# Performance work log

Hardware: AMD Instinct MI355X
Metric: run time of the kernel (lower is better)

## Reference

```python
import jax, jax.numpy as jnp
import numpy as np

BN_EPS = 1e-5

def _conv3x3(x, w):
    # x: [N,C,H,W], w: [O,I,3,3], stride 1, padding 1, no bias
    return jax.lax.conv_general_dilated(
        x, w, window_strides=(1, 1), padding=((1, 1), (1, 1)),
        dimension_numbers=("NCHW", "OIHW", "NCHW"))

def _batchnorm(x, gamma, beta):
    # training-mode BN: batch statistics over (N,H,W)
    mean = jnp.mean(x, axis=(0, 2, 3), keepdims=True)
    var = jnp.mean(jnp.square(x - mean), axis=(0, 2, 3), keepdims=True)
    inv = jax.lax.rsqrt(var + BN_EPS)
    g = gamma.reshape(1, -1, 1, 1)
    b = beta.reshape(1, -1, 1, 1)
    return (x - mean) * inv * g + b

def setup_inputs() -> dict:
    key = jax.random.key(0)
    ks = jax.random.split(key, 3)
    x = jax.random.normal(ks[0], (32, 64, 128, 128), dtype=jnp.float32)
    # He-style scaled 3x3 conv kernels
    w1 = jax.random.normal(ks[1], (64, 64, 3, 3), dtype=jnp.float32) * (2.0 / (64 * 9)) ** 0.5
    w2 = jax.random.normal(ks[2], (64, 64, 3, 3), dtype=jnp.float32) * (2.0 / (64 * 9)) ** 0.5
    return {
        "x": x, "w1": w1, "w2": w2,
        "bn1_gamma": jnp.ones((64,), jnp.float32),
        "bn1_beta": jnp.zeros((64,), jnp.float32),
        "bn2_gamma": jnp.ones((64,), jnp.float32),
        "bn2_beta": jnp.zeros((64,), jnp.float32),
    }

def reference(x, w1, w2, bn1_gamma, bn1_beta, bn2_gamma, bn2_beta):
    out = _batchnorm(_conv3x3(x, w1), bn1_gamma, bn1_beta)
    out = _conv3x3(out, w2)
    out = out + x  # option 'A', stride=1, planes[2]==planes[0] -> identity shortcut
    return _batchnorm(out, bn2_gamma, bn2_beta)
```

## Files before the change

### kernel.cpp

```cpp
#include <hip/hip_runtime.h>
#include <hip/hip_bf16.h>

#define NB 32
#define CH 64
#define HH 128
#define WW 128
#define HW (HH*WW)
#define CHW (CH*HW)
#define NCHW (NB*CHW)
#define CNT_PER_CH ((float)(NB*HW))
#define SLOTS 256

typedef __attribute__((ext_vector_type(8)))  short short8;
typedef __attribute__((ext_vector_type(16))) float f32x16;

__device__ __forceinline__ unsigned short f2bf(float f) {
  unsigned u = __builtin_bit_cast(unsigned, f);
  u += 0x7fffu + ((u >> 16) & 1u);
  return (unsigned short)(u >> 16);
}

__device__ __forceinline__ void gld_lds16(const void* g, void* s) {
  __builtin_amdgcn_global_load_lds(
      (const __attribute__((address_space(1))) unsigned int*)g,
      (__attribute__((address_space(3))) unsigned int*)s, 16, 0, 0);
}

__global__ __launch_bounds__(256) void t1_pack(const float* __restrict__ x,
                                               unsigned short* __restrict__ xb) {
  __shared__ __align__(16) unsigned short tmp[CH * WW];
  const int bid = blockIdx.x;
  const int tid = threadIdx.x;
  const float* src = x + (size_t)(bid >> 7) * CHW + (size_t)(bid & 127) * WW;
  for (int i = tid; i < 2048; i += 256) {
    const int ci = i >> 5, wq = i & 31;
    const float4 v = *(const float4*)(src + (size_t)ci * HW + wq * 4);
    unsigned short* d = &tmp[ci * WW + wq * 4];
    d[0] = f2bf(v.x); d[1] = f2bf(v.y); d[2] = f2bf(v.z); d[3] = f2bf(v.w);
  }
  __syncthreads();
  unsigned short* dst = xb + (size_t)bid * 8192;
  for (int i = tid; i < 1024; i += 256) {
    const int cb = i >> 7, w = i & 127;
    const unsigned short* s = &tmp[cb * 8 * WW + w];
    uint4 o;
    o.x = (unsigned)s[0]      | ((unsigned)s[WW]     << 16);
    o.y = (unsigned)s[2*WW]   | ((unsigned)s[3*WW]   << 16);
    o.z = (unsigned)s[4*WW]   | ((unsigned)s[5*WW]   << 16);
    o.w = (unsigned)s[6*WW]   | ((unsigned)s[7*WW]   << 16);
    *(uint4*)(dst + ((size_t)cb * WW + w) * 8) = o;
  }
}

__global__ __launch_bounds__(256) void pack_w(const float* __restrict__ w,
                                              const float* __restrict__ s1,
                                              const float* __restrict__ b1,
                                              unsigned short* __restrict__ wpk,
                                              float* __restrict__ tabs) {
  const int tid = threadIdx.x;
  for (int idx = tid; idx < 36864; idx += 256) {
    const int f = idx >> 9, l = (idx >> 3) & 63, r = idx & 7;
    const int m = f & 1, kq = (f >> 1) & 3, t = f >> 3;
    const int co = (l & 31) + 32 * m;
    const int ci = kq * 16 + (l >> 5) * 8 + r;
    float v = w[co * 576 + ci * 9 + t];
    if (s1) v *= s1[ci];
    wpk[idx] = f2bf(v);
  }
  if (tabs != nullptr && tid < 64) {
    const int co = tid;
    float tb[9];
    for (int t = 0; t < 9; ++t) {
      float a = 0.f;
      for (int ci = 0; ci < 64; ++ci) a += w[co * 576 + ci * 9 + t] * b1[ci];
      tb[t] = a;
    }
    tabs[0*64+co] = tb[0]+tb[1]+tb[2]+tb[3]+tb[4]+tb[5]+tb[6]+tb[7]+tb[8];
    tabs[1*64+co] = tb[0]+tb[1]+tb[2];
    tabs[2*64+co] = tb[6]+tb[7]+tb[8];
    tabs[3*64+co] = tb[0]+tb[3]+tb[6];
    tabs[4*64+co] = tb[2]+tb[5]+tb[8];
    tabs[5*64+co] = tb[0]; tabs[6*64+co] = tb[2];
    tabs[7*64+co] = tb[6]; tabs[8*64+co] = tb[8];
  }
}

template <bool IS2>
__global__ __launch_bounds__(256, 2)
void conv_tile(const unsigned short* __restrict__ inb,
               const unsigned short* __restrict__ wpack,
               const float* __restrict__ tabs,
               const float* __restrict__ resid,
               unsigned short* __restrict__ outb,
               float* __restrict__ outf,
               float* __restrict__ psum, float* __restrict__ psq) {
  __shared__ __align__(16) unsigned short A[4][8][128][8];
  const int b = blockIdx.x;
  const int vid = ((b & 7) << 8) | (b >> 3);
  const int n  = vid >> 6;
  const int h0 = (vid & 63) << 1;
  const int tid = threadIdx.x;
  const int wv = tid >> 6, lane = tid & 63;
  const int half = lane >> 5, lp = lane & 31;
  const int m   = wv & 1;
  const int row = wv >> 1;
  const int rrow = h0 + row;

  short8 wr[36];
#pragma unroll
  for (int i = 0; i < 36; ++i) {
    const int f = (i << 1) + m;
    wr[i] = *(const short8*)(wpack + ((size_t)f << 9) + ((size_t)lane << 3));
  }

#pragma unroll
  for (int t = 0; t < 16; ++t) {
    const int task = wv + (t << 2);
    const int ri = task >> 4, cb = (task >> 1) & 7, wh = task & 1;
    const int hr = h0 - 1 + ri;
    if ((unsigned)hr < 128u) {
      const unsigned short* g = inb + ((((size_t)n * 128 + hr) * 8 + cb) << 10)
                                    + (size_t)((wh << 6) + lane) * 8;
      gld_lds16(g, &A[ri][cb][wh << 6][0]);
    } else {
      *(uint4*)&A[ri][cb][(wh << 6) + lane][0] = make_uint4(0, 0, 0, 0);
    }
  }
  __syncthreads();

  f32x16 acc[4] = {{}, {}, {}, {}};
#pragma unroll
  for (int kh = 0; kh < 3; ++kh) {
    const int ri = row + kh;
#pragma unroll
    for (int kw = 0; kw < 3; ++kw) {
#pragma unroll
      for (int kq = 0; kq < 4; ++kq) {
        const short8 wf = wr[(kh * 3 + kw) * 4 + kq];
        const int cb = (kq << 1) + half;
#pragma unroll
        for (int seg = 0; seg < 4; ++seg) {
          const int ps = (seg << 5) + lp + kw - 1;
          int pc = ps;
          bool zero = false;
          if (kw == 0 && seg == 0) { pc = ps < 0 ? 0 : ps; zero = ps < 0; }
          if (kw == 2 && seg == 3) { pc = ps > 127 ? 127 : ps; zero = ps > 127; }
          short8 bf = *(const short8*)&A[ri][cb][pc][0];
          if ((kw == 0 && seg == 0) || (kw == 2 && seg == 3)) {
            short8 zz = {};
            if (zero) bf = zz;
          }
          acc[seg] = __builtin_amdgcn_mfma_f32_32x32x16_bf16(wf, bf, acc[seg], 0, 0, 0);
        }
      }
    }
  }

  if (!IS2) {
    unsigned short* dst = outb + (size_t)(n * 128 + rrow) * 8192;
#pragma unroll
    for (int seg = 0; seg < 4; ++seg) {
      const f32x16& a = acc[seg];
      const int px = (seg << 5) + lp;
#pragma unroll
      for (int rq = 0; rq < 4; ++rq) {
        uint2 pk;
        pk.x = (unsigned)f2bf(a[rq*4+0]) | ((unsigned)f2bf(a[rq*4+1]) << 16);
        pk.y = (unsigned)f2bf(a[rq*4+2]) | ((unsigned)f2bf(a[rq*4+3]) << 16);
        *(uint2*)(dst + (((size_t)(rq + (m << 2))) << 10) + ((size_t)px << 3) + (half << 2)) = pk;
      }
    }
  } else {
    const bool bh0 = (rrow == 0), bh1 = (rrow == 127);
#pragma unroll
    for (int seg = 0; seg < 4; ++seg) {
      f32x16& a = acc[seg];
      const int px = (seg << 5) + lp;
      const bool bw0 = (px == 0), bw1 = (px == 127);
#pragma unroll
      for (int r = 0; r < 16; ++r) {
        const int co = (r & 3) + ((r >> 2) << 3) + (half << 2) + (m << 5);
        float tb = tabs[co];
        if (bh0) tb -= tabs[64 + co];
        if (bh1) tb -= tabs[128 + co];
        if (bw0) tb -= tabs[192 + co];
        if (bw1) tb -= tabs[256 + co];
        if (bh0 && bw0) tb += tabs[320 + co];
        if (bh0 && bw1) tb += tabs[384 + co];
        if (bh1 && bw0) tb += tabs[448 + co];
        if (bh1 && bw1) tb += tabs[512 + co];
        const size_t oi = (((size_t)(n * 64 + co)) * 128 + rrow) * 128 + px;
        const float v = a[r] + tb + resid[oi];
        outf[oi] = v;
        a[r] = v;
      }
    }
  }

  const int slot = vid & (SLOTS - 1);
#pragma unroll
  for (int r = 0; r < 16; ++r) {
    float s = acc[0][r] + acc[1][r] + acc[2][r] + acc[3][r];
    float q = acc[0][r]*acc[0][r] + acc[1][r]*acc[1][r]
            + acc[2][r]*acc[2][r] + acc[3][r]*acc[3][r];
    s += __shfl_xor(s, 1);  q += __shfl_xor(q, 1);
    s += __shfl_xor(s, 2);  q += __shfl_xor(q, 2);
    s += __shfl_xor(s, 4);  q += __shfl_xor(q, 4);
    s += __shfl_xor(s, 8);  q += __shfl_xor(q, 8);
    s += __shfl_xor(s, 16); q += __shfl_xor(q, 16);
    if (lp == 0) {
      const int co = (r & 3) + ((r >> 2) << 3) + (half << 2) + (m << 5);
      atomicAdd(&psum[slot * 64 + co], s);
      atomicAdd(&psq [slot * 64 + co], q);
    }
  }
}

__global__ __launch_bounds__(256)
void finalize_bn(const float* __restrict__ psum, const float* __restrict__ psq,
                 const float* __restrict__ gamma, const float* __restrict__ beta,
                 float* __restrict__ scale, float* __restrict__ bias) {
  __shared__ float ls[4][64], lq[4][64];
  const int c = threadIdx.x & 63, sg = threadIdx.x >> 6;
  float s = 0.f, q = 0.f;
  for (int i = sg * (SLOTS / 4); i < (sg + 1) * (SLOTS / 4); ++i) {
    s += psum[(size_t)i * 64 + c];
    q += psq[(size_t)i * 64 + c];
  }
  ls[sg][c] = s; lq[sg][c] = q;
  __syncthreads();
  if (threadIdx.x < 64) {
    s = ls[0][c] + ls[1][c] + ls[2][c] + ls[3][c];
    q = lq[0][c] + lq[1][c] + lq[2][c] + lq[3][c];
    const float mean = s * (1.0f / CNT_PER_CH);
    const float var  = q * (1.0f / CNT_PER_CH) - mean * mean;
    const float inv  = rsqrtf(var + 1e-5f);
    const float sc   = inv * gamma[c];
    scale[c] = sc;
    bias[c]  = beta[c] - mean * sc;
  }
}

__global__ __launch_bounds__(256)
void apply_bn_k(float* __restrict__ out,
                const float* __restrict__ scale, const float* __restrict__ bias) {
  __shared__ float sc[CH], bs[CH];
  if (threadIdx.x < CH) { sc[threadIdx.x] = scale[threadIdx.x]; bs[threadIdx.x] = bias[threadIdx.x]; }
  __syncthreads();
  const size_t total4 = NCHW / 4;
  for (size_t i = (size_t)blockIdx.x * blockDim.x + threadIdx.x; i < total4;
       i += (size_t)gridDim.x * blockDim.x) {
    float4 v = reinterpret_cast<float4*>(out)[i];
    const int c = (int)(((i * 4) >> 14) & 63);
    const float s = sc[c], b = bs[c];
    v.x = fmaf(v.x, s, b);
    v.y = fmaf(v.y, s, b);
    v.z = fmaf(v.z, s, b);
    v.w = fmaf(v.w, s, b);
    reinterpret_cast<float4*>(out)[i] = v;
  }
}

extern "C" void kernel_launch(void* const* d_in, const int* in_sizes, int n_in,
                              void* d_out, int out_size, void* d_ws, size_t ws_size,
                              hipStream_t stream) {
  const float* x  = (const float*)d_in[0];
  const float* w1 = (const float*)d_in[1];
  const float* w2 = (const float*)d_in[2];
  const float* g1 = (const float*)d_in[3];
  const float* b1 = (const float*)d_in[4];
  const float* g2 = (const float*)d_in[5];
  const float* b2 = (const float*)d_in[6];
  float* out = (float*)d_out;
  char* ws = (char*)d_ws;

  unsigned short* XB  = (unsigned short*)ws;
  unsigned short* Y1B = (unsigned short*)(ws + 67108864);
  unsigned short* W2P = (unsigned short*)ws;
  float* TABS = (float*)(ws + 73728);
  float* SC1  = (float*)(ws + 76032);
  float* BS1  = (float*)(ws + 76288);
  float* SC2  = (float*)(ws + 76544);
  float* BS2  = (float*)(ws + 76800);
  float* P2S  = (float*)(ws + 131072);
  float* P2Q  = (float*)(ws + 131072 + 65536);
  char* ob = (char*)d_out;
  unsigned short* W1P = (unsigned short*)ob;
  float* P1S = (float*)(ob + 73728);
  float* P1Q = (float*)(ob + 73728 + 65536);

  pack_w<<<1, 256, 0, stream>>>(w1, nullptr, nullptr, W1P, nullptr);
  hipMemsetAsync(ob + 73728, 0, 131072, stream);
  t1_pack<<<4096, 256, 0, stream>>>(x, XB);
  conv_tile<false><<<2048, 256, 0, stream>>>(XB, W1P, nullptr, nullptr,
                                             Y1B, nullptr, P1S, P1Q);
  finalize_bn<<<1, 256, 0, stream>>>(P1S, P1Q, g1, b1, SC1, BS1);
  hipMemsetAsync(ws + 131072, 0, 131072, stream);
  pack_w<<<1, 256, 0, stream>>>(w2, SC1, BS1, W2P, TABS);
  conv_tile<true><<<2048, 256, 0, stream>>>(Y1B, W2P, TABS, x,
                                            nullptr, out, P2S, P2Q);
  finalize_bn<<<1, 256, 0, stream>>>(P2S, P2Q, g2, b2, SC2, BS2);
  apply_bn_k<<<2048, 256, 0, stream>>>(out, SC2, BS2);
}
```

Measured before the change: 573.9 us.

## Stage conv weights in LDS and split pixel segments across 512-thread blocks

The conv kernel used to hold all 36 weight fragments in registers per wave and run 4 accumulators per wave. Weights are now loaded into dynamic shared memory (72 KB) alongside the input tile, and the block doubles to 8 waves, each covering two of the four 32-pixel segments. This cuts register pressure, allowing more waves in flight. In exchange it adds an LDS read per MFMA for the weights, and the larger LDS footprint (about 104 KB per block) may limit how many blocks fit per CU.

```diff
diff --git a/kernel.cpp b/kernel.cpp
--- a/kernel.cpp
+++ b/kernel.cpp
@@ -86,7 +86,7 @@
 }
 
 template <bool IS2>
-__global__ __launch_bounds__(256, 2)
+__global__ __launch_bounds__(512, 2)
 void conv_tile(const unsigned short* __restrict__ inb,
                const unsigned short* __restrict__ wpack,
                const float* __restrict__ tabs,
@@ -94,7 +94,8 @@
                unsigned short* __restrict__ outb,
                float* __restrict__ outf,
                float* __restrict__ psum, float* __restrict__ psq) {
-  __shared__ __align__(16) unsigned short A[4][8][128][8];
+  __shared__ __align__(16) unsigned short A[4 * 8 * 128 * 8];
+  extern __shared__ __align__(16) unsigned short WL[];
   const int b = blockIdx.x;
   const int vid = ((b & 7) << 8) | (b >> 3);
   const int n  = vid >> 6;
@@ -102,33 +103,34 @@
   const int tid = threadIdx.x;
   const int wv = tid >> 6, lane = tid & 63;
   const int half = lane >> 5, lp = lane & 31;
-  const int m   = wv & 1;
-  const int row = wv >> 1;
+  const int row = wv & 1;
+  const int m   = (wv >> 1) & 1;
+  const int sh  = wv >> 2;
   const int rrow = h0 + row;
 
-  short8 wr[36];
-#pragma unroll
-  for (int i = 0; i < 36; ++i) {
-    const int f = (i << 1) + m;
-    wr[i] = *(const short8*)(wpack + ((size_t)f << 9) + ((size_t)lane << 3));
-  }
-
-#pragma unroll
-  for (int t = 0; t < 16; ++t) {
-    const int task = wv + (t << 2);
-    const int ri = task >> 4, cb = (task >> 1) & 7, wh = task & 1;
-    const int hr = h0 - 1 + ri;
-    if ((unsigned)hr < 128u) {
-      const unsigned short* g = inb + ((((size_t)n * 128 + hr) * 8 + cb) << 10)
-                                    + (size_t)((wh << 6) + lane) * 8;
-      gld_lds16(g, &A[ri][cb][wh << 6][0]);
-    } else {
-      *(uint4*)&A[ri][cb][(wh << 6) + lane][0] = make_uint4(0, 0, 0, 0);
+#pragma unroll
+  for (int i = 0; i < 17; ++i) {
+    const int t = wv + (i << 3);
+    if (t < 64) {
+      const int ri = t >> 4, cb = (t >> 1) & 7, wh = t & 1;
+      const int hr = h0 - 1 + ri;
+      if ((unsigned)hr < 128u) {
+        const unsigned short* g = inb + ((((size_t)n * 128 + hr) * 8 + cb) << 10)
+                                      + (size_t)((wh << 6) + lane) * 8;
+        gld_lds16(g, &A[(((ri * 8 + cb) << 7) + (wh << 6)) << 3]);
+      } else {
+        *(uint4*)&A[(((ri * 8 + cb) << 7) + (wh << 6) + lane) << 3] =
+            make_uint4(0, 0, 0, 0);
+      }
+    } else if (t < 136) {
+      const int f = t - 64;
+      const unsigned short* g = wpack + ((size_t)f << 9) + ((size_t)lane << 3);
+      gld_lds16(g, &WL[f << 9]);
     }
   }
   __syncthreads();
 
-  f32x16 acc[4] = {{}, {}, {}, {}};
+  f32x16 acc0 = {}; f32x16 acc1 = {};
 #pragma unroll
   for (int kh = 0; kh < 3; ++kh) {
     const int ri = row + kh;
@@ -136,21 +138,24 @@
     for (int kw = 0; kw < 3; ++kw) {
 #pragma unroll
       for (int kq = 0; kq < 4; ++kq) {
-        const short8 wf = wr[(kh * 3 + kw) * 4 + kq];
+        const int f = (((kh * 3 + kw) << 2) + kq) << 1 | m;
+        const short8 wf = *(const short8*)&WL[(f << 9) + (lane << 3)];
         const int cb = (kq << 1) + half;
-#pragma unroll
-        for (int seg = 0; seg < 4; ++seg) {
-          const int ps = (seg << 5) + lp + kw - 1;
+        const unsigned short* base = &A[((ri * 8 + cb) << 10)];
+#pragma unroll
+        for (int s = 0; s < 2; ++s) {
+          const int ps = (((sh << 1) + s) << 5) + lp + kw - 1;
           int pc = ps;
-          bool zero = false;
-          if (kw == 0 && seg == 0) { pc = ps < 0 ? 0 : ps; zero = ps < 0; }
-          if (kw == 2 && seg == 3) { pc = ps > 127 ? 127 : ps; zero = ps > 127; }
-          short8 bf = *(const short8*)&A[ri][cb][pc][0];
-          if ((kw == 0 && seg == 0) || (kw == 2 && seg == 3)) {
+          bool ze = false;
+          if (kw == 0 && s == 0) { pc = ps < 0 ? 0 : ps; ze = (sh == 0) && (ps < 0); }
+          if (kw == 2 && s == 1) { pc = ps > 127 ? 127 : ps; ze = (sh == 1) && (ps > 127); }
+          short8 bf = *(const short8*)&base[pc << 3];
+          if ((kw == 0 && s == 0) || (kw == 2 && s == 1)) {
             short8 zz = {};
-            if (zero) bf = zz;
+            if (ze) bf = zz;
           }
-          acc[seg] = __builtin_amdgcn_mfma_f32_32x32x16_bf16(wf, bf, acc[seg], 0, 0, 0);
+          if (s == 0) acc0 = __builtin_amdgcn_mfma_f32_32x32x16_bf16(wf, bf, acc0, 0, 0, 0);
+          else        acc1 = __builtin_amdgcn_mfma_f32_32x32x16_bf16(wf, bf, acc1, 0, 0, 0);
         }
       }
     }
@@ -159,9 +164,9 @@
   if (!IS2) {
     unsigned short* dst = outb + (size_t)(n * 128 + rrow) * 8192;
 #pragma unroll
-    for (int seg = 0; seg < 4; ++seg) {
-      const f32x16& a = acc[seg];
-      const int px = (seg << 5) + lp;
+    for (int s = 0; s < 2; ++s) {
+      const f32x16& a = s ? acc1 : acc0;
+      const int px = (((sh << 1) + s) << 5) + lp;
 #pragma unroll
       for (int rq = 0; rq < 4; ++rq) {
         uint2 pk;
@@ -173,9 +178,9 @@
   } else {
     const bool bh0 = (rrow == 0), bh1 = (rrow == 127);
 #pragma unroll
-    for (int seg = 0; seg < 4; ++seg) {
-      f32x16& a = acc[seg];
-      const int px = (seg << 5) + lp;
+    for (int s = 0; s < 2; ++s) {
+      f32x16& a = s ? acc1 : acc0;
+      const int px = (((sh << 1) + s) << 5) + lp;
       const bool bw0 = (px == 0), bw1 = (px == 127);
 #pragma unroll
       for (int r = 0; r < 16; ++r) {
@@ -200,9 +205,8 @@
   const int slot = vid & (SLOTS - 1);
 #pragma unroll
   for (int r = 0; r < 16; ++r) {
-    float s = acc[0][r] + acc[1][r] + acc[2][r] + acc[3][r];
-    float q = acc[0][r]*acc[0][r] + acc[1][r]*acc[1][r]
-            + acc[2][r]*acc[2][r] + acc[3][r]*acc[3][r];
+    float s = acc0[r] + acc1[r];
+    float q = acc0[r] * acc0[r] + acc1[r] * acc1[r];
     s += __shfl_xor(s, 1);  q += __shfl_xor(q, 1);
     s += __shfl_xor(s, 2);  q += __shfl_xor(q, 2);
     s += __shfl_xor(s, 4);  q += __shfl_xor(q, 4);
@@ -289,16 +293,18 @@
   float* P1S = (float*)(ob + 73728);
   float* P1Q = (float*)(ob + 73728 + 65536);
 
+  const size_t wlds = 73728;
+
   pack_w<<<1, 256, 0, stream>>>(w1, nullptr, nullptr, W1P, nullptr);
   hipMemsetAsync(ob + 73728, 0, 131072, stream);
   t1_pack<<<4096, 256, 0, stream>>>(x, XB);
-  conv_tile<false><<<2048, 256, 0, stream>>>(XB, W1P, nullptr, nullptr,
-                                             Y1B, nullptr, P1S, P1Q);
+  conv_tile<false><<<2048, 512, wlds, stream>>>(XB, W1P, nullptr, nullptr,
+                                                Y1B, nullptr, P1S, P1Q);
   finalize_bn<<<1, 256, 0, stream>>>(P1S, P1Q, g1, b1, SC1, BS1);
   hipMemsetAsync(ws + 131072, 0, 131072, stream);
   pack_w<<<1, 256, 0, stream>>>(w2, SC1, BS1, W2P, TABS);
-  conv_tile<true><<<2048, 256, 0, stream>>>(Y1B, W2P, TABS, x,
-                                            nullptr, out, P2S, P2Q);
+  conv_tile<true><<<2048, 512, wlds, stream>>>(Y1B, W2P, TABS, x,
+                                               nullptr, out, P2S, P2Q);
   finalize_bn<<<1, 256, 0, stream>>>(P2S, P2Q, g2, b2, SC2, BS2);
   apply_bn_k<<<2048, 256, 0, stream>>>(out, SC2, BS2);
 }
```

Measured after the change: 619.0 us. 1.08x slower.
